# Performance work log

Measured on AMD Instinct MI355X. Metric: run time of the kernel, lower is better.

The kernel has to match this reference:

```python
import jax, jax.numpy as jnp
import numpy as np

FIELD = 7  # field_size


def _conv1x1(x, w):
    # x: [b,c,h,w], w: [c_out,c_in] (1x1 conv, no bias)
    return jnp.einsum('bchw,oc->bohw', x, w)


def _patches(x, f):
    # torch unfold with 'same' padding: output [b, c*f*f, h, w], channel-major
    # (feature index = c*f*f + kh*f + kw), matching KAIR extract_image_patches
    # layout for odd f / stride 1 (symmetric pad (f-1)//2).
    return jax.lax.conv_general_dilated_patches(
        x, filter_shape=(f, f), window_strides=(1, 1), padding='SAME',
        dimension_numbers=('NCHW', 'OIHW', 'NCHW'))


def setup_inputs() -> dict:
    key = jax.random.key(0)
    k0, k1, k2, k3, k4 = jax.random.split(key, 5)
    c, ci = 256, 128
    b, h, w = 4, 64, 64
    s = 1.0 / np.sqrt(c)
    si = 1.0 / np.sqrt(ci)
    return {
        'x': jax.random.normal(k0, (b, c, h, w), dtype=jnp.float32),
        'w_phi': jax.random.normal(k1, (ci, c), dtype=jnp.float32) * s,
        'w_theta': jax.random.normal(k2, (ci, c), dtype=jnp.float32) * s,
        'w_g': jax.random.normal(k3, (ci, c), dtype=jnp.float32) * s,
        'w_mask': jax.random.normal(k4, (c, ci), dtype=jnp.float32) * si,
    }


def reference(x, w_phi, w_theta, w_g, w_mask):
    b, c, h, w = x.shape
    ci = w_phi.shape[0]
    f = FIELD
    kk = f * f

    x_phi = _conv1x1(x, w_phi)      # [b,ci,h,w]
    x_g = _conv1x1(x, w_g)          # [b,ci,h,w]
    x_theta = _conv1x1(x, w_theta)  # [b,ci,h,w]

    # theta: unsqueeze(-2) then permute(0,2,4,3,1) -> [b,h,w,1,ci]
    q = jnp.transpose(x_theta, (0, 2, 3, 1))[:, :, :, None, :]

    # phi patches: [b, ci*kk, h, w] reshaped (row-major, faithful to torch
    # reshape of the unfold output) to [b,h,w,ci,kk]
    p_phi = _patches(x_phi, f).reshape(b, h, w, ci, kk)
    scores = jnp.matmul(q, p_phi)                 # [b,h,w,1,kk]
    attn = jax.nn.softmax(scores, axis=1)         # softmax over dim=1 (h), faithful

    p_g = _patches(x_g, f).reshape(b, h, w, kk, ci)
    out = jnp.matmul(attn, p_g)                   # [b,h,w,1,ci]

    # permute(0,4,3,1,2).view(b,ci,h,w)
    y = jnp.transpose(out, (0, 4, 3, 1, 2)).reshape(b, ci, h, w)
    mask = _conv1x1(y, w_mask)                    # [b,c,h,w]
    return mask + x
```

## Files before the change

kernel.cpp:

```cpp
#include <hip/hip_runtime.h>


#define PLANE    5040
#define A_BATCH  645120

typedef __attribute__((ext_vector_type(8))) short short8;
typedef __attribute__((ext_vector_type(4))) float floatx4;

__device__ __forceinline__ float bf2f(unsigned short u) {
    union { unsigned int i; float f; } v; v.i = ((unsigned int)u) << 16; return v.f;
}
__device__ __forceinline__ unsigned short f2bf(float f) {
    union { float f; unsigned int i; } v; v.f = f;
    unsigned int r = v.i + 0x7FFFu + ((v.i >> 16) & 1u);
    return (unsigned short)(r >> 16);
}

__global__ __launch_bounds__(256) void prep_kernel(
    const float* __restrict__ x,
    const float* __restrict__ w_phi,
    const float* __restrict__ w_theta,
    const float* __restrict__ w_g,
    const float* __restrict__ w_mask,
    unsigned short* __restrict__ xp_hi,
    unsigned short* __restrict__ xp_lo,
    unsigned short* __restrict__ w3p_hi,
    unsigned short* __restrict__ w3p_lo,
    unsigned short* __restrict__ wmp_hi,
    unsigned short* __restrict__ wmp_lo,
    uint4* __restrict__ zero_region)
{
    const int tid = threadIdx.x;
    const int bx = blockIdx.x;

    if (bx < 1024) {
        const int b  = bx >> 8;
        const int kt = (bx >> 6) & 3;
        const int pt = bx & 63;
        __shared__ float tile[64][65];
        #pragma unroll
        for (int i = 0; i < 16; ++i) {
            int lin = tid + i * 256;
            int kk = lin >> 6, pp = lin & 63;
            tile[kk][pp] = x[(b * 256 + kt * 64 + kk) * 4096 + pt * 64 + pp];
        }
        __syncthreads();
        #pragma unroll
        for (int i = 0; i < 16; ++i) {
            int lin = tid + i * 256;
            int frag = lin >> 9;
            int idx  = lin & 511;
            int kbL  = frag >> 2;
            int ptL  = frag & 3;
            int j    = idx & 7;
            int n    = (idx >> 3) & 15;
            int quad = idx >> 7;
            float f = tile[kbL * 32 + quad * 8 + j][ptL * 16 + n];
            unsigned short h = f2bf(f);
            int addr = ((b * 8 + kt * 2 + kbL) * 256 + pt * 4 + ptL) * 512 + idx;
            xp_hi[addr] = h;
            xp_lo[addr] = f2bf(f - bf2f(h));
        }
    } else {
        const int wid = (bx - 1024) * 256 + tid;
        for (int e = wid; e < 98304; e += 32768) {
            int frag = e >> 9;
            int idx  = e & 511;
            int nt16 = frag >> 3, kb = frag & 7;
            int j = idx & 7, m = (idx >> 3) & 15, quad = idx >> 7;
            int n = nt16 * 16 + m;
            int k = kb * 32 + quad * 8 + j;
            float v = (n < 128) ? w_phi[n * 256 + k]
                    : (n < 256) ? w_theta[(n - 128) * 256 + k]
                                : w_g[(n - 256) * 256 + k];
            unsigned short h = f2bf(v);
            w3p_hi[e] = h;
            w3p_lo[e] = f2bf(v - bf2f(h));
        }
        {
            int e = wid;
            int frag = e >> 9;
            int idx  = e & 511;
            int ot16 = frag >> 2, kb = frag & 3;
            int j = idx & 7, m = (idx >> 3) & 15, quad = idx >> 7;
            float v = w_mask[(ot16 * 16 + m) * 128 + kb * 32 + quad * 8 + j];
            unsigned short h = f2bf(v);
            wmp_hi[e] = h;
            wmp_lo[e] = f2bf(v - bf2f(h));
        }
        const uint4 z = make_uint4(0u, 0u, 0u, 0u);
        for (int i = wid; i < 645120; i += 32768) zero_region[i] = z;
    }
}

__global__ __launch_bounds__(256) void conv3_mfma_kernel(
    const unsigned short* __restrict__ xp_hi,
    const unsigned short* __restrict__ xp_lo,
    const unsigned short* __restrict__ w3p_hi,
    const unsigned short* __restrict__ w3p_lo,
    unsigned short* __restrict__ A_phi,
    unsigned short* __restrict__ theta_bf,
    unsigned short* __restrict__ A_g)
{
    const int tid = threadIdx.x;
    const int w   = tid >> 6;
    const int ln  = tid & 63;
    const int lm  = ln & 15;
    const int quad = ln >> 4;
    const int bx = blockIdx.x;
    const int nt = blockIdx.y;
    const int b  = blockIdx.z;
    const int nt16a = nt * 8 + w;
    const int nt16b = nt * 8 + 4 + w;
    const int lnofs = ln * 8;

    floatx4 accA[4] = {{0.f,0.f,0.f,0.f},{0.f,0.f,0.f,0.f},
                       {0.f,0.f,0.f,0.f},{0.f,0.f,0.f,0.f}};
    floatx4 accB[4] = {{0.f,0.f,0.f,0.f},{0.f,0.f,0.f,0.f},
                       {0.f,0.f,0.f,0.f},{0.f,0.f,0.f,0.f}};

    #pragma unroll
    for (int kb = 0; kb < 8; ++kb) {
        const int aoffA = (nt16a * 8 + kb) * 512 + lnofs;
        const int aoffB = (nt16b * 8 + kb) * 512 + lnofs;
        const int boff  = ((b * 8 + kb) * 256 + bx * 4) * 512 + lnofs;
        short8 ahA = *reinterpret_cast<const short8*>(w3p_hi + aoffA);
        short8 alA = *reinterpret_cast<const short8*>(w3p_lo + aoffA);
        short8 ahB = *reinterpret_cast<const short8*>(w3p_hi + aoffB);
        short8 alB = *reinterpret_cast<const short8*>(w3p_lo + aoffB);
        short8 bh[4], bl[4];
        #pragma unroll
        for (int ct = 0; ct < 4; ++ct) {
            bh[ct] = *reinterpret_cast<const short8*>(xp_hi + boff + ct * 512);
            bl[ct] = *reinterpret_cast<const short8*>(xp_lo + boff + ct * 512);
        }
        #pragma unroll
        for (int ct = 0; ct < 4; ++ct) {
            accA[ct] = __builtin_amdgcn_mfma_f32_16x16x32_bf16(ahA, bh[ct], accA[ct], 0, 0, 0);
            accA[ct] = __builtin_amdgcn_mfma_f32_16x16x32_bf16(ahA, bl[ct], accA[ct], 0, 0, 0);
            accA[ct] = __builtin_amdgcn_mfma_f32_16x16x32_bf16(alA, bh[ct], accA[ct], 0, 0, 0);
            accB[ct] = __builtin_amdgcn_mfma_f32_16x16x32_bf16(ahB, bh[ct], accB[ct], 0, 0, 0);
            accB[ct] = __builtin_amdgcn_mfma_f32_16x16x32_bf16(ahB, bl[ct], accB[ct], 0, 0, 0);
            accB[ct] = __builtin_amdgcn_mfma_f32_16x16x32_bf16(alB, bh[ct], accB[ct], 0, 0, 0);
        }
    }

    const int py = bx;
    if (nt == 1) {
        #pragma unroll
        for (int ct = 0; ct < 4; ++ct) {
            const int p = bx * 64 + ct * 16 + lm;
            #pragma unroll
            for (int reg = 0; reg < 4; ++reg) {
                const int r = w * 16 + quad * 4 + reg;
                theta_bf[(b * 4096 + p) * 128 + r]      = f2bf(accA[ct][reg]);
                theta_bf[(b * 4096 + p) * 128 + r + 64] = f2bf(accB[ct][reg]);
            }
        }
    } else {
        unsigned short* __restrict__ A = (nt == 0) ? A_phi : A_g;
        #pragma unroll
        for (int ct = 0; ct < 4; ++ct) {
            const int pxx = ct * 16 + lm;
            #pragma unroll
            for (int reg = 0; reg < 4; ++reg) {
                const int r = w * 16 + quad * 4 + reg;
                A[b * A_BATCH + r * PLANE + (py + 3) * 72 + pxx + 4] =
                    f2bf(accA[ct][reg]);
                A[b * A_BATCH + (r + 64) * PLANE + (py + 3) * 72 + pxx + 4] =
                    f2bf(accB[ct][reg]);
            }
        }
    }
}

__global__ __launch_bounds__(256) void scores_kernel(
    const unsigned short* __restrict__ Apad,
    const unsigned short* __restrict__ theta_bf,
    float* __restrict__ scores)
{
    const int w  = threadIdx.x >> 6;
    const int ln = threadIdx.x & 63;
    const int s  = blockIdx.x * 4 + w;
    const int b  = blockIdx.y;

    __shared__ float th[4][128];
    {
        const unsigned short* tb = theta_bf + (b * 4096 + s) * 128;
        th[w][ln]      = bf2f(tb[ln]);
        th[w][ln + 64] = bf2f(tb[ln + 64]);
    }
    __syncthreads();

    const unsigned short* __restrict__ Ab = Apad + b * A_BATCH;

    const int base  = s * 6272;
    const int ch_lo = base >> 12;
    const unsigned B1 = (unsigned)(ch_lo + 1) << 12;
    const unsigned B2 = (unsigned)(ch_lo + 2) << 12;
    const int d1 = (int)B1 - base;
    const int d2 = d1 + 4096;

    int A1 = d1 / 49;
    int A2 = (d1 + 48) / 49;
    int C1 = d2 / 49;        if (C1 > 128) C1 = 128;
    int C2 = (d2 + 48) / 49; if (C2 > 128) C2 = 128;

    unsigned OFFv[3];
    #pragma unroll
    for (int i = 0; i < 3; ++i) {
        int ch = ch_lo + i;
        int c0 = ch / 49; if (c0 > 127) c0 = 127;
        int rr = ch - c0 * 49;
        int kh = rr / 7;
        int kw = rr - kh * 7;
        OFFv[i] = (unsigned)(c0 * PLANE + kh * 72 + kw + 1);
    }

    unsigned F = (unsigned)(base + ln);
    float acc = 0.f;

    {
        const unsigned OFF_ = OFFv[0];
        #pragma unroll 4
        for (int cc = 0; cc < A1; ++cc) {
            unsigned p = F & 4095u;
            unsigned a = OFF_ + p + ((p >> 6) << 3);
            acc = fmaf(th[w][cc], bf2f(Ab[a]), acc);
            F += 49u;
        }
    }
    for (int cc = A1; cc < A2; ++cc) {
        unsigned OFF_ = (F >= B1) ? OFFv[1] : OFFv[0];
        unsigned p = F & 4095u;
        unsigned a = OFF_ + p + ((p >> 6) << 3);
        acc = fmaf(th[w][cc], bf2f(Ab[a]), acc);
        F += 49u;
    }
    {
        const unsigned OFF_ = OFFv[1];
        #pragma unroll 4
        for (int cc = A2; cc < C1; ++cc) {
            unsigned p = F & 4095u;
            unsigned a = OFF_ + p + ((p >> 6) << 3);
            acc = fmaf(th[w][cc], bf2f(Ab[a]), acc);
            F += 49u;
        }
    }
    for (int cc = C1; cc < C2; ++cc) {
        unsigned OFF_ = (F >= B2) ? OFFv[2] : OFFv[1];
        unsigned p = F & 4095u;
        unsigned a = OFF_ + p + ((p >> 6) << 3);
        acc = fmaf(th[w][cc], bf2f(Ab[a]), acc);
        F += 49u;
    }
    {
        const unsigned OFF_ = OFFv[2];
        #pragma unroll 4
        for (int cc = C2; cc < 128; ++cc) {
            unsigned p = F & 4095u;
            unsigned a = OFF_ + p + ((p >> 6) << 3);
            acc = fmaf(th[w][cc], bf2f(Ab[a]), acc);
            F += 49u;
        }
    }

    if (ln < 49) scores[(b * 4096 + s) * 64 + ln] = acc;
}

__global__ __launch_bounds__(256) void softmax_stats_kernel(
    const float* __restrict__ scores,
    float* __restrict__ m_arr,
    float* __restrict__ inv_arr)
{
    const int b = blockIdx.x >> 6;
    const int j = blockIdx.x & 63;
    const int tid = threadIdx.x;
    const int wv = tid >> 6;
    const int ln = tid & 63;

    __shared__ float tile[64][52];

    #pragma unroll
    for (int it = 0; it < 16; ++it) {
        int i = it * 4 + wv;
        if (ln < 49) tile[i][ln] = scores[(b * 4096 + i * 64 + j) * 64 + ln];
    }
    __syncthreads();

    if (tid < 49) {
        float m = -3.4e38f;
        #pragma unroll 8
        for (int i = 0; i < 64; ++i) m = fmaxf(m, tile[i][tid]);
        float sum = 0.f;
        #pragma unroll 8
        for (int i = 0; i < 64; ++i) sum += __expf(tile[i][tid] - m);
        m_arr[(b * 64 + j) * 49 + tid]   = m;
        inv_arr[(b * 64 + j) * 49 + tid] = 1.f / sum;
    }
}

__global__ __launch_bounds__(512) void agg_mask_kernel(
    const float* __restrict__ scores,
    const float* __restrict__ m_arr,
    const float* __restrict__ inv_arr,
    const unsigned short* __restrict__ Apad,
    const unsigned short* __restrict__ wmp_hi,
    const unsigned short* __restrict__ wmp_lo,
    const float* __restrict__ x,
    float* __restrict__ out)
{
    const int tid = threadIdx.x;
    const int blk = blockIdx.x;
    const int b   = blockIdx.y;
    const int P0  = blk * 32;

    __shared__ float at_l[32][52];
    __shared__ unsigned short y_lds[8 * 512];

    const int j0 = P0 & 63;
    #pragma unroll
    for (int it = 0; it < 4; ++it) {
        int idx = tid + it * 512;
        int lp = idx >> 6;
        int t  = idx & 63;
        if (t < 49) {
            const int s = P0 + lp;
            const int j = j0 + lp;
            float sc = scores[(b * 4096 + s) * 64 + t];
            float m  = m_arr[(b * 64 + j) * 49 + t];
            float iv = inv_arr[(b * 64 + j) * 49 + t];
            at_l[lp][t] = __expf(sc - m) * iv;
        }
    }
    __syncthreads();

    const unsigned short* __restrict__ Ab = Apad + b * A_BATCH;
    const int pq = tid >> 7;
    const int cc = tid & 127;

    #pragma unroll
    for (int rep = 0; rep < 8; ++rep) {
        const int lp = rep * 4 + pq;
        const int s  = P0 + lp;

        const int base  = s * 6272;
        const int ch_lo = base >> 12;
        const unsigned B1 = (unsigned)(ch_lo + 1) << 12;
        const unsigned B2 = (unsigned)(ch_lo + 2) << 12;
        const int d1 = (int)B1 - base;
        const int d2 = d1 + 4096;

        int A1 = d1 >> 7;
        int A2 = (d1 + 127) >> 7;
        int C1 = d2 >> 7;          if (C1 > 49) C1 = 49;
        int C2 = (d2 + 127) >> 7;  if (C2 > 49) C2 = 49;
        if (A1 > 49) A1 = 49;
        if (A2 > 49) A2 = 49;

        unsigned OFFv[3];
        #pragma unroll
        for (int i = 0; i < 3; ++i) {
            int ch = ch_lo + i;
            int c0 = ch / 49; if (c0 > 127) c0 = 127;
            int rr = ch - c0 * 49;
            int kh = rr / 7;
            int kw = rr - kh * 7;
            OFFv[i] = (unsigned)(c0 * PLANE + kh * 72 + kw + 1);
        }

        unsigned F = (unsigned)(base + cc);
        float acc = 0.f;

        {
            const unsigned OFF_ = OFFv[0];
            #pragma unroll 4
            for (int t = 0; t < A1; ++t) {
                unsigned p = F & 4095u;
                unsigned a = OFF_ + p + ((p >> 6) << 3);
                acc = fmaf(at_l[lp][t], bf2f(Ab[a]), acc);
                F += 128u;
            }
        }
        for (int t = A1; t < A2; ++t) {
            unsigned OFF_ = (F >= B1) ? OFFv[1] : OFFv[0];
            unsigned p = F & 4095u;
            unsigned a = OFF_ + p + ((p >> 6) << 3);
            acc = fmaf(at_l[lp][t], bf2f(Ab[a]), acc);
            F += 128u;
        }
        {
            const unsigned OFF_ = OFFv[1];
            #pragma unroll 4
            for (int t = A2; t < C1; ++t) {
                unsigned p = F & 4095u;
                unsigned a = OFF_ + p + ((p >> 6) << 3);
                acc = fmaf(at_l[lp][t], bf2f(Ab[a]), acc);
                F += 128u;
            }
        }
        for (int t = C1; t < C2; ++t) {
            unsigned OFF_ = (F >= B2) ? OFFv[2] : OFFv[1];
            unsigned p = F & 4095u;
            unsigned a = OFF_ + p + ((p >> 6) << 3);
            acc = fmaf(at_l[lp][t], bf2f(Ab[a]), acc);
            F += 128u;
        }
        {
            const unsigned OFF_ = OFFv[2];
            for (int t = C2; t < 49; ++t) {
                unsigned p = F & 4095u;
                unsigned a = OFF_ + p + ((p >> 6) << 3);
                acc = fmaf(at_l[lp][t], bf2f(Ab[a]), acc);
                F += 128u;
            }
        }

        const int kb = cc >> 5, k32 = cc & 31;
        const int quad = k32 >> 3, jx = k32 & 7;
        const int ct = lp >> 4, n = lp & 15;
        y_lds[(kb * 2 + ct) * 512 + (quad * 16 + n) * 8 + jx] = f2bf(acc);
    }
    __syncthreads();

    const int w    = tid >> 6;
    const int ln   = tid & 63;
    const int lm   = ln & 15;
    const int quad = ln >> 4;
    const int lnofs = ln * 8;
    const int ot16a = w;
    const int ot16b = w + 8;

    floatx4 accA[2] = {{0.f,0.f,0.f,0.f},{0.f,0.f,0.f,0.f}};
    floatx4 accB[2] = {{0.f,0.f,0.f,0.f},{0.f,0.f,0.f,0.f}};

    #pragma unroll
    for (int kb = 0; kb < 4; ++kb) {
        const int aoffA = (ot16a * 4 + kb) * 512 + lnofs;
        const int aoffB = (ot16b * 4 + kb) * 512 + lnofs;
        short8 ahA = *reinterpret_cast<const short8*>(wmp_hi + aoffA);
        short8 alA = *reinterpret_cast<const short8*>(wmp_lo + aoffA);
        short8 ahB = *reinterpret_cast<const short8*>(wmp_hi + aoffB);
        short8 alB = *reinterpret_cast<const short8*>(wmp_lo + aoffB);
        short8 bf[2];
        #pragma unroll
        for (int ct = 0; ct < 2; ++ct)
            bf[ct] = *reinterpret_cast<const short8*>(
                y_lds + (kb * 2 + ct) * 512 + lnofs);
        #pragma unroll
        for (int ct = 0; ct < 2; ++ct) {
            accA[ct] = __builtin_amdgcn_mfma_f32_16x16x32_bf16(ahA, bf[ct], accA[ct], 0, 0, 0);
            accA[ct] = __builtin_amdgcn_mfma_f32_16x16x32_bf16(alA, bf[ct], accA[ct], 0, 0, 0);
            accB[ct] = __builtin_amdgcn_mfma_f32_16x16x32_bf16(ahB, bf[ct], accB[ct], 0, 0, 0);
            accB[ct] = __builtin_amdgcn_mfma_f32_16x16x32_bf16(alB, bf[ct], accB[ct], 0, 0, 0);
        }
    }

    #pragma unroll
    for (int ct = 0; ct < 2; ++ct) {
        const int p = P0 + ct * 16 + lm;
        #pragma unroll
        for (int reg = 0; reg < 4; ++reg) {
            const int oA = w * 16 + quad * 4 + reg;
            const int ofsA = (b * 256 + oA) * 4096 + p;
            out[ofsA] = accA[ct][reg] + x[ofsA];
            const int ofsB = ofsA + 128 * 4096;
            out[ofsB] = accB[ct][reg] + x[ofsB];
        }
    }
}

extern "C" void kernel_launch(void* const* d_in, const int* in_sizes, int n_in,
                              void* d_out, int out_size, void* d_ws, size_t ws_size,
                              hipStream_t stream) {
    const float* x       = (const float*)d_in[0];
    const float* w_phi   = (const float*)d_in[1];
    const float* w_theta = (const float*)d_in[2];
    const float* w_g     = (const float*)d_in[3];
    const float* w_mask  = (const float*)d_in[4];

    float* out_f = (float*)d_out;

    unsigned short* ws_u  = (unsigned short*)d_ws;
    unsigned short* A_phi = ws_u;
    unsigned short* A_g   = ws_u + 2580480;
    unsigned short* th_u  = ws_u + 7258112;
    float*          sc_f  = (float*)(ws_u + 9355264);
    unsigned short* xph   = ws_u + 11452416;
    unsigned short* xpl   = ws_u + 15646720;
    unsigned short* w3ph  = ws_u + 19841024;
    unsigned short* w3pl  = ws_u + 19939328;
    unsigned short* wmph  = ws_u + 20037632;
    unsigned short* wmpl  = ws_u + 20070400;
    float*          m_f   = (float*)(ws_u + 20103168);
    float*          inv_f = (float*)(ws_u + 20128256);

    hipLaunchKernelGGL(prep_kernel, dim3(1152), dim3(256), 0, stream,
                       x, w_phi, w_theta, w_g, w_mask,
                       xph, xpl, w3ph, w3pl, wmph, wmpl, (uint4*)A_phi);
    hipLaunchKernelGGL(conv3_mfma_kernel, dim3(64, 3, 4), dim3(256), 0, stream,
                       xph, xpl, w3ph, w3pl, A_phi, th_u, A_g);
    hipLaunchKernelGGL(scores_kernel, dim3(1024, 4), dim3(256), 0, stream,
                       A_phi, th_u, sc_f);
    hipLaunchKernelGGL(softmax_stats_kernel, dim3(256), dim3(256), 0, stream,
                       sc_f, m_f, inv_f);
    hipLaunchKernelGGL(agg_mask_kernel, dim3(128, 4), dim3(512), 0, stream,
                       sc_f, m_f, inv_f, A_g, wmph, wmpl, x, out_f);
}
```

Measured before the change: 174.3 us.

## Double agg_mask block size and strength-reduce patch address computation

```diff
diff --git a/kernel.cpp b/kernel.cpp
--- a/kernel.cpp
+++ b/kernel.cpp
@@ -300,7 +300,7 @@
     }
 }
 
-__global__ __launch_bounds__(512) void agg_mask_kernel(
+__global__ __launch_bounds__(1024) void agg_mask_kernel(
     const float* __restrict__ scores,
     const float* __restrict__ m_arr,
     const float* __restrict__ inv_arr,
@@ -320,8 +320,8 @@
 
     const int j0 = P0 & 63;
     #pragma unroll
-    for (int it = 0; it < 4; ++it) {
-        int idx = tid + it * 512;
+    for (int it = 0; it < 2; ++it) {
+        int idx = tid + it * 1024;
         int lp = idx >> 6;
         int t  = idx & 63;
         if (t < 49) {
@@ -340,8 +340,8 @@
     const int cc = tid & 127;
 
     #pragma unroll
-    for (int rep = 0; rep < 8; ++rep) {
-        const int lp = rep * 4 + pq;
+    for (int rep = 0; rep < 4; ++rep) {
+        const int lp = rep * 8 + pq;
         const int s  = P0 + lp;
 
         const int base  = s * 6272;
@@ -369,50 +369,49 @@
             OFFv[i] = (unsigned)(c0 * PLANE + kh * 72 + kw + 1);
         }
 
-        unsigned F = (unsigned)(base + cc);
         float acc = 0.f;
 
         {
-            const unsigned OFF_ = OFFv[0];
+            unsigned p0 = (unsigned)(base + cc) & 4095u;
+            unsigned a = OFFv[0] + p0 + ((p0 >> 6) << 3);
             #pragma unroll 4
             for (int t = 0; t < A1; ++t) {
-                unsigned p = F & 4095u;
-                unsigned a = OFF_ + p + ((p >> 6) << 3);
                 acc = fmaf(at_l[lp][t], bf2f(Ab[a]), acc);
-                F += 128u;
+                a += 144u;
             }
         }
         for (int t = A1; t < A2; ++t) {
+            unsigned F = (unsigned)(base + cc) + 128u * (unsigned)t;
             unsigned OFF_ = (F >= B1) ? OFFv[1] : OFFv[0];
             unsigned p = F & 4095u;
             unsigned a = OFF_ + p + ((p >> 6) << 3);
             acc = fmaf(at_l[lp][t], bf2f(Ab[a]), acc);
-            F += 128u;
         }
         {
-            const unsigned OFF_ = OFFv[1];
+            unsigned F = (unsigned)(base + cc) + 128u * (unsigned)A2;
+            unsigned p0 = F & 4095u;
+            unsigned a = OFFv[1] + p0 + ((p0 >> 6) << 3);
             #pragma unroll 4
             for (int t = A2; t < C1; ++t) {
-                unsigned p = F & 4095u;
-                unsigned a = OFF_ + p + ((p >> 6) << 3);
                 acc = fmaf(at_l[lp][t], bf2f(Ab[a]), acc);
-                F += 128u;
+                a += 144u;
             }
         }
         for (int t = C1; t < C2; ++t) {
+            unsigned F = (unsigned)(base + cc) + 128u * (unsigned)t;
             unsigned OFF_ = (F >= B2) ? OFFv[2] : OFFv[1];
             unsigned p = F & 4095u;
             unsigned a = OFF_ + p + ((p >> 6) << 3);
             acc = fmaf(at_l[lp][t], bf2f(Ab[a]), acc);
-            F += 128u;
         }
         {
-            const unsigned OFF_ = OFFv[2];
+            unsigned F = (unsigned)(base + cc) + 128u * (unsigned)C2;
+            unsigned p0 = F & 4095u;
+            unsigned a = OFFv[2] + p0 + ((p0 >> 6) << 3);
+            #pragma unroll 4
             for (int t = C2; t < 49; ++t) {
-                unsigned p = F & 4095u;
-                unsigned a = OFF_ + p + ((p >> 6) << 3);
                 acc = fmaf(at_l[lp][t], bf2f(Ab[a]), acc);
-                F += 128u;
+                a += 144u;
             }
         }
 
@@ -428,20 +427,14 @@
     const int lm   = ln & 15;
     const int quad = ln >> 4;
     const int lnofs = ln * 8;
-    const int ot16a = w;
-    const int ot16b = w + 8;
 
     floatx4 accA[2] = {{0.f,0.f,0.f,0.f},{0.f,0.f,0.f,0.f}};
-    floatx4 accB[2] = {{0.f,0.f,0.f,0.f},{0.f,0.f,0.f,0.f}};
 
     #pragma unroll
     for (int kb = 0; kb < 4; ++kb) {
-        const int aoffA = (ot16a * 4 + kb) * 512 + lnofs;
-        const int aoffB = (ot16b * 4 + kb) * 512 + lnofs;
+        const int aoffA = (w * 4 + kb) * 512 + lnofs;
         short8 ahA = *reinterpret_cast<const short8*>(wmp_hi + aoffA);
         short8 alA = *reinterpret_cast<const short8*>(wmp_lo + aoffA);
-        short8 ahB = *reinterpret_cast<const short8*>(wmp_hi + aoffB);
-        short8 alB = *reinterpret_cast<const short8*>(wmp_lo + aoffB);
         short8 bf[2];
         #pragma unroll
         for (int ct = 0; ct < 2; ++ct)
@@ -451,8 +444,6 @@
         for (int ct = 0; ct < 2; ++ct) {
             accA[ct] = __builtin_amdgcn_mfma_f32_16x16x32_bf16(ahA, bf[ct], accA[ct], 0, 0, 0);
             accA[ct] = __builtin_amdgcn_mfma_f32_16x16x32_bf16(alA, bf[ct], accA[ct], 0, 0, 0);
-            accB[ct] = __builtin_amdgcn_mfma_f32_16x16x32_bf16(ahB, bf[ct], accB[ct], 0, 0, 0);
-            accB[ct] = __builtin_amdgcn_mfma_f32_16x16x32_bf16(alB, bf[ct], accB[ct], 0, 0, 0);
         }
     }
 
@@ -464,8 +455,6 @@
             const int oA = w * 16 + quad * 4 + reg;
             const int ofsA = (b * 256 + oA) * 4096 + p;
             out[ofsA] = accA[ct][reg] + x[ofsA];
-            const int ofsB = ofsA + 128 * 4096;
-            out[ofsB] = accB[ct][reg] + x[ofsB];
         }
     }
 }
@@ -504,6 +493,6 @@
                        A_phi, th_u, sc_f);
     hipLaunchKernelGGL(softmax_stats_kernel, dim3(256), dim3(256), 0, stream,
                        sc_f, m_f, inv_f);
-    hipLaunchKernelGGL(agg_mask_kernel, dim3(128, 4), dim3(512), 0, stream,
+    hipLaunchKernelGGL(agg_mask_kernel, dim3(128, 4), dim3(1024), 0, stream,
                        sc_f, m_f, inv_f, A_g, wmph, wmpl, x, out_f);
 }
```

Measured after the change: 162.6 us. 1.07x faster.
